# Kernel tuning notes

Measured on AMD Instinct MI355X. Metric: run time of the kernel, lower is better.

## Reference

```python
import jax, jax.numpy as jnp
import numpy as np
import math

R = 16            # input_resolution (window side)
N = R * R         # tokens per window
H = 16            # num_heads
D = 32            # head_dim
SCALE = D ** -0.5

def _rel_pos_index(r):
    # Swin-style relative position index, [N, N] int
    coords = np.stack(np.meshgrid(np.arange(r), np.arange(r), indexing='ij'))  # [2,r,r]
    cf = coords.reshape(2, -1)                          # [2, N]
    rel = cf[:, :, None] - cf[:, None, :]               # [2, N, N]
    rel = rel.transpose(1, 2, 0).astype(np.int64)       # [N, N, 2]
    rel[:, :, 0] += r - 1
    rel[:, :, 1] += r - 1
    rel[:, :, 0] *= 2 * r - 1
    return rel.sum(-1)                                  # [N, N]

def _modulation(n, k):
    # cosine-distance modulation matrix, [n*n, n*n]
    idx = np.arange(n * n)
    rr, cc = idx // n, idx % n
    d = np.sqrt((rr[:, None] - rr[None, :]) ** 2 + (cc[:, None] - cc[None, :]) ** 2)
    T = 4 * (n - 1) * math.sqrt(2)
    f = 2 * math.pi / T
    m = np.exp(np.cos(f * d)) / 2
    if k % n == 0:
        k = k - 1
    bound = m[0, k]
    m = np.where(m < bound, 0.0, m)
    return jnp.asarray(m, jnp.float32)

_REL_IDX = jnp.asarray(_rel_pos_index(R))   # [N, N] int
_MOD = _modulation(R, 3 * R)                 # [N, N] float (eval-mode local modulation)

def setup_inputs() -> dict:
    key = jax.random.key(0)
    ks = jax.random.split(key, 6)
    C = H * D
    return {
        'x': jax.random.normal(ks[0], (128, N, C), jnp.float32),
        'qkv_w': jax.random.normal(ks[1], (3 * C, C), jnp.float32) * 0.02,
        'qkv_b': jax.random.normal(ks[2], (3 * C,), jnp.float32) * 0.02,
        'proj_w': jax.random.normal(ks[3], (C, C), jnp.float32) * 0.02,
        'proj_b': jax.random.normal(ks[4], (C,), jnp.float32) * 0.02,
        'rpb_table': jax.random.normal(ks[5], ((2 * R - 1) ** 2, H), jnp.float32) * 0.02,
    }

def reference(x, qkv_w, qkv_b, proj_w, proj_b, rpb_table):
    B, n, C = x.shape
    # qkv projection: torch Linear is x @ W^T + b
    qkv = x @ qkv_w.T + qkv_b                       # [B, N, 3C]
    qkv = qkv.reshape(B, n, 3, H, D)
    q = qkv[:, :, 0].transpose(0, 2, 1, 3) * SCALE  # [B, H, N, D]
    k = qkv[:, :, 1].transpose(0, 2, 1, 3)
    v = qkv[:, :, 2].transpose(0, 2, 1, 3)
    attn = jnp.einsum('bhnd,bhmd->bhnm', q, k)      # [B, H, N, N]
    bias = rpb_table[_REL_IDX]                      # [N, N, H]
    attn = attn + bias.transpose(2, 0, 1)[None]     # + [1, H, N, N]
    attn = jax.nn.softmax(attn, axis=-1)
    attn = attn * _MOD[None, None]                  # local eval-mode modulation
    out = jnp.einsum('bhnm,bhmd->bhnd', attn, v)    # [B, H, N, D]
    out = out.transpose(0, 2, 1, 3).reshape(B, n, C)
    return out @ proj_w.T + proj_b
```

## Files before the change

kernel.cpp:

```cpp
#include <hip/hip_runtime.h>
#include <hip/hip_bf16.h>

typedef unsigned short u16;
typedef unsigned int u32;
typedef __bf16 bf16x8 __attribute__((ext_vector_type(8)));
typedef float f32x4 __attribute__((ext_vector_type(4)));

#define AS1(p) ((const __attribute__((address_space(1))) void*)(p))
#define AS3(p) ((__attribute__((address_space(3))) void*)(p))

#define TOK   256
#define CDIM  512
#define QKVC  1536
#define LOG2E 1.4426950408889634f
#define QSCALE (0.17677669529663687f * 1.4426950408889634f)

__device__ __forceinline__ u16 f2b(float f) {
  unsigned u = __float_as_uint(f);
  unsigned r = (u + 0x7fffu + ((u >> 16) & 1u)) >> 16;
  return (u16)r;
}
__device__ __forceinline__ u16 f2bc(float f) {
  __bf16 h = (__bf16)f;
  u16 u;
  __builtin_memcpy(&u, &h, 2);
  return u;
}
__device__ __forceinline__ float bf_lo(u32 wd) { return __uint_as_float(wd << 16); }
__device__ __forceinline__ float bf_hi(u32 wd) { return __uint_as_float(wd & 0xffff0000u); }
__device__ __forceinline__ float ex2(float x) {
  float r;
  asm("v_exp_f32 %0, %1" : "=v"(r) : "v"(x));
  return r;
}

__global__ __launch_bounds__(256) void cvt_bf16_kernel(const float* __restrict__ in,
                                                       u16* __restrict__ out, int n) {
  int i = (blockIdx.x * 256 + threadIdx.x) * 8;
  if (i >= n) return;
  float4 a = *(const float4*)(in + i);
  float4 b = *(const float4*)(in + i + 4);
  u16 h[8];
  h[0] = f2b(a.x); h[1] = f2b(a.y); h[2] = f2b(a.z); h[3] = f2b(a.w);
  h[4] = f2b(b.x); h[5] = f2b(b.y); h[6] = f2b(b.z); h[7] = f2b(b.w);
  *(uint4*)(out + i) = *(const uint4*)h;
}

__global__ __launch_bounds__(256) void build_bias2_kernel(const float* __restrict__ rpb,
                                                          u16* __restrict__ bias2) {
  int i = blockIdx.x * 256 + threadIdx.x;
  int tr = i & 63, lane = (i >> 6) & 63, rb = (i >> 12) & 15, h = i >> 16;
  int t = tr >> 2, r = tr & 3;
  int n = rb * 16 + (lane & 15);
  int m = t * 16 + (lane >> 4) * 4 + r;
  int idx = ((n >> 4) - (m >> 4) + 15) * 31 + ((n & 15) - (m & 15) + 15);
  bias2[i] = f2b(rpb[idx * 16 + h] * LOG2E);
}

__global__ __launch_bounds__(256) void build_mod2_kernel(u16* __restrict__ mod2) {
  int i = blockIdx.x * 256 + threadIdx.x;
  int tr = i & 63, lane = (i >> 6) & 63, rb = i >> 12;
  int t = tr >> 2, r = tr & 3;
  int n = rb * 16 + (lane & 15);
  int m = t * 16 + (lane >> 4) * 4 + r;
  int dr = (n >> 4) - (m >> 4), dc = (n & 15) - (m & 15);
  int d2 = dr * dr + dc * dc;
  float val = 0.0f;
  if (d2 <= 229) {
    const float fc = 6.2831853071795864f / (60.0f * 1.4142135623730951f);
    val = expf(cosf(fc * sqrtf((float)d2))) * 0.5f;
  }
  mod2[i] = f2b(val);
}

template<int MODE>
__global__ __launch_bounds__(256) void gemm_bt(const u16* __restrict__ A,
                                               const u16* __restrict__ Bt,
                                               const float* __restrict__ bvec,
                                               u16* __restrict__ oq,
                                               u16* __restrict__ ok,
                                               u16* __restrict__ ov,
                                               float* __restrict__ of) {
  constexpr int K = 512;
  constexpr int NBN = (MODE == 0) ? 12 : 4;
  constexpr int PER_XCD = (MODE == 0) ? 384 : 128;
  __shared__ __align__(16) u16 As[128 * 64];
  __shared__ __align__(16) u16 Bs[128 * 64];
  const int tid = threadIdx.x, lane = tid & 63, w = tid >> 6;
  const int wr = w >> 1, wc = w & 1, lr = lane & 15, lg = lane >> 4;
  const int logical = (blockIdx.x & 7) * PER_XCD + (blockIdx.x >> 3);
  const int bm = (logical / (2 * NBN)) * 2 + (logical & 1);
  const int bn = (logical % (2 * NBN)) >> 1;
  const u16* Ag = A + (size_t)bm * 128 * K;
  const u16* Bg = Bt + (size_t)bn * 128 * K;
  f32x4 acc[4][4];
#pragma unroll
  for (int m = 0; m < 4; ++m)
#pragma unroll
    for (int n = 0; n < 4; ++n) acc[m][n] = (f32x4){0.f, 0.f, 0.f, 0.f};

  for (int k0 = 0; k0 < K; k0 += 64) {
#pragma unroll
    for (int it = 0; it < 4; ++it) {
      int chunk = it * 256 + w * 64 + lane;
      int r = chunk >> 3, kc = chunk & 7;
      int kcs = kc ^ (r & 7);
      __builtin_amdgcn_global_load_lds(AS1(Ag + (size_t)r * K + k0 + kcs * 8),
                                       AS3(As + chunk * 8), 16, 0, 0);
      __builtin_amdgcn_global_load_lds(AS1(Bg + (size_t)r * K + k0 + kcs * 8),
                                       AS3(Bs + chunk * 8), 16, 0, 0);
    }
    __syncthreads();
#pragma unroll
    for (int kk = 0; kk < 2; ++kk) {
      bf16x8 a[4], b[4];
#pragma unroll
      for (int m = 0; m < 4; ++m) {
        int ar = wr * 64 + m * 16 + lr;
        a[m] = *(const bf16x8*)&As[ar * 64 + (((kk * 4 + lg) ^ (lr & 7)) << 3)];
      }
#pragma unroll
      for (int n = 0; n < 4; ++n) {
        int br = wc * 64 + n * 16 + lr;
        b[n] = *(const bf16x8*)&Bs[br * 64 + (((kk * 4 + lg) ^ (lr & 7)) << 3)];
      }
#pragma unroll
      for (int m = 0; m < 4; ++m)
#pragma unroll
        for (int n = 0; n < 4; ++n)
          acc[m][n] = __builtin_amdgcn_mfma_f32_16x16x32_bf16(a[m], b[n], acc[m][n], 0, 0, 0);
    }
    __syncthreads();
  }

  if (MODE == 1) {
#pragma unroll
    for (int m = 0; m < 4; ++m)
#pragma unroll
      for (int n = 0; n < 4; ++n)
#pragma unroll
        for (int r = 0; r < 4; ++r) {
          int row = bm * 128 + wr * 64 + m * 16 + lg * 4 + r;
          int col = bn * 128 + wc * 64 + n * 16 + lr;
          of[(size_t)row * CDIM + col] = acc[m][n][r] + bvec[col];
        }
    return;
  }

  const int typ = bn >> 2;
  const int col0 = bn * 128 + wc * 64;
  const int row0 = bm * 128 + wr * 64;
  char* Tb = (char*)((w < 2 ? As : Bs) + (w & 1) * 4096);

#pragma unroll
  for (int n = 0; n < 4; ++n) {
    float bv = bvec[col0 + n * 16 + lr];
#pragma unroll
    for (int m = 0; m < 4; ++m)
#pragma unroll
      for (int r = 0; r < 4; ++r) {
        float v = acc[m][n][r] + bv;
        if (typ == 0) v *= QSCALE;
        int row_l, col_l;
        if (typ < 2) { row_l = m * 16 + lg * 4 + r; col_l = n * 16 + lr; }
        else         { row_l = n * 16 + lr;         col_l = m * 16 + lg * 4 + r; }
        int byte = row_l * 128 + ((((col_l >> 3) ^ (row_l & 7)) << 4) | ((col_l & 7) << 1));
        *(u16*)(Tb + byte) = f2b(v);
      }
  }
  asm volatile("" ::: "memory");
  if (typ < 2) {
    int tok = row0 + lane;
    int tokb = tok >> 8;
    u16* obase = (typ == 0) ? oq : ok;
#pragma unroll
    for (int G = 0; G < 8; ++G) {
      int hl = G >> 2, q = G & 3;
      uint4 v = *(const uint4*)(Tb + lane * 128 + ((G ^ (lane & 7)) << 4));
      int hh = ((col0 >> 5) & 15) + hl;
      size_t a = ((((size_t)tokb * 16 + hh) * 16 + ((tok >> 4) & 15)) * 64 +
                  ((tok & 15) | (q << 4))) * 8;
      *(uint4*)(obase + a) = v;
    }
  } else {
    int tl0 = row0 & 255, tokb = row0 >> 8;
    int hl = lane >> 5, t = (lane >> 3) & 3, c = lane & 7;
    int hh = ((col0 >> 5) & 15) + hl;
#pragma unroll
    for (int i = 0; i < 8; ++i) {
      int d = i * 4 + t;
      uint4 v = *(const uint4*)(Tb + (hl * 32 + d) * 128 + (c << 4));
      size_t a = (((size_t)tokb * 16 + hh) * 32 + d) * 256 + tl0 + c * 8;
      *(uint4*)(ov + a) = v;
    }
  }
}

__global__ __launch_bounds__(512, 4) void attn_kernel(const u16* __restrict__ qfrag,
                                                      const u16* __restrict__ kfrag,
                                                      const u16* __restrict__ vsw,
                                                      const u16* __restrict__ bias2,
                                                      const u16* __restrict__ mod2,
                                                      u16* __restrict__ attnout) {
  __shared__ __align__(16) u16 SM[24576];
  const int logical = (blockIdx.x & 7) * 512 + (blockIdx.x >> 3);
  const int h = logical >> 8;
  const int b = (logical >> 1) & 127;
  const int qpair = logical & 1;
  const int tid = threadIdx.x, lane = tid & 63, w = tid >> 6;
  const int lr = lane & 15, lg = lane >> 4;
  const int rb = qpair * 8 + w;
  const int bhid = b * 16 + h;

  const u16* kg = kfrag + (size_t)bhid * 8192;
  const u16* vg = vsw + (size_t)bhid * 8192;
#pragma unroll
  for (int it = 0; it < 2; ++it) {
    __builtin_amdgcn_global_load_lds(AS1(kg + (it * 512 + tid) * 8),
                                     AS3(SM + (it * 512 + tid) * 8), 16, 0, 0);
    __builtin_amdgcn_global_load_lds(AS1(vg + (it * 512 + tid) * 8),
                                     AS3(SM + 8192 + (it * 512 + tid) * 8), 16, 0, 0);
  }
  bf16x8 qf = *(const bf16x8*)(qfrag + ((size_t)bhid * 16 + rb) * 512 + lane * 8);
  __syncthreads();

  const u16* bias_base = bias2 + (((size_t)h * 16 + rb) * 64 + lane) * 64;
  const u16* mod_base  = mod2 + ((size_t)rb * 64 + lane) * 64;
  char* Pbase = (char*)SM + 32768 + w * 2048;
  const char* Vb = (const char*)(SM + 8192);

  f32x4 s[16];
#pragma unroll
  for (int q = 0; q < 4; ++q) {
    u32 bw8[8];
    {
      const uint4* bp = (const uint4*)(bias_base + q * 16);
      *(uint4*)&bw8[0] = bp[0]; *(uint4*)&bw8[4] = bp[1];
    }
#pragma unroll
    for (int tl = 0; tl < 4; ++tl) {
      int t = q * 4 + tl;
      bf16x8 kf = *(const bf16x8*)(SM + (t * 64 + lane) * 8);
      f32x4 c;
      c[0] = bf_lo(bw8[tl * 2]);     c[1] = bf_hi(bw8[tl * 2]);
      c[2] = bf_lo(bw8[tl * 2 + 1]); c[3] = bf_hi(bw8[tl * 2 + 1]);
      s[t] = __builtin_amdgcn_mfma_f32_16x16x32_bf16(kf, qf, c, 0, 0, 0);
    }
  }

  float mr0 = s[0][0], mr1 = s[0][1], mr2 = s[0][2], mr3 = s[0][3];
#pragma unroll
  for (int t = 1; t < 16; ++t) {
    mr0 = fmaxf(mr0, s[t][0]); mr1 = fmaxf(mr1, s[t][1]);
    mr2 = fmaxf(mr2, s[t][2]); mr3 = fmaxf(mr3, s[t][3]);
  }
  float mx = fmaxf(fmaxf(mr0, mr1), fmaxf(mr2, mr3));
  mx = fmaxf(mx, __shfl_xor(mx, 16, 64));
  mx = fmaxf(mx, __shfl_xor(mx, 32, 64));
  float s0 = 0.f, s1 = 0.f, s2 = 0.f, s3 = 0.f;
#pragma unroll
  for (int t = 0; t < 16; ++t) {
    s[t][0] = ex2(s[t][0] - mx); s0 += s[t][0];
    s[t][1] = ex2(s[t][1] - mx); s1 += s[t][1];
    s[t][2] = ex2(s[t][2] - mx); s2 += s[t][2];
    s[t][3] = ex2(s[t][3] - mx); s3 += s[t][3];
  }
  float sm = (s0 + s1) + (s2 + s3);
  sm += __shfl_xor(sm, 16, 64);
  sm += __shfl_xor(sm, 32, 64);
  sm = __builtin_amdgcn_rcpf(sm);

  f32x4 o0 = (f32x4){0.f, 0.f, 0.f, 0.f};
  f32x4 o1 = (f32x4){0.f, 0.f, 0.f, 0.f};
#pragma unroll
  for (int q = 0; q < 4; ++q) {
    u32 mw8[8];
    {
      const uint4* mp = (const uint4*)(mod_base + q * 16);
      *(uint4*)&mw8[0] = mp[0]; *(uint4*)&mw8[4] = mp[1];
    }
#pragma unroll
    for (int tl = 0; tl < 4; ++tl) {
      int t = q * 4 + tl;
      u16 pk[4];
#pragma unroll
      for (int r = 0; r < 4; ++r) {
        u32 wd = mw8[tl * 2 + (r >> 1)];
        float mf = (r & 1) ? bf_hi(wd) : bf_lo(wd);
        pk[r] = f2bc(s[t][r] * sm * mf);
      }
      int hi2 = (t * 2 + (lg >> 1)) & 3;
      *(uint2*)(Pbase + ((t >> 1) & 1) * 1024 + ((hi2 << 4) | lr) * 16 + (lg & 1) * 8)
          = *(const uint2*)pk;
    }
    asm volatile("" ::: "memory");
#pragma unroll
    for (int kl = 0; kl < 2; ++kl) {
      bf16x8 pa = *(const bf16x8*)(Pbase + kl * 1024 + lane * 16);
      int cv = ((q * 2 + kl) * 4 + lg) ^ (lr & 7);
      bf16x8 v0 = *(const bf16x8*)(Vb + lr * 512 + cv * 16);
      bf16x8 v1 = *(const bf16x8*)(Vb + (16 + lr) * 512 + cv * 16);
      o0 = __builtin_amdgcn_mfma_f32_16x16x32_bf16(pa, v0, o0, 0, 0, 0);
      o1 = __builtin_amdgcn_mfma_f32_16x16x32_bf16(pa, v1, o1, 0, 0, 0);
    }
    asm volatile("" ::: "memory");
  }

  u16* orow = attnout + (size_t)(b * TOK + rb * 16) * CDIM + h * 32;
#pragma unroll
  for (int r = 0; r < 4; ++r) {
    orow[(size_t)(lg * 4 + r) * CDIM + lr] = f2bc(o0[r]);
    orow[(size_t)(lg * 4 + r) * CDIM + 16 + lr] = f2bc(o1[r]);
  }
}

extern "C" void kernel_launch(void* const* d_in, const int* in_sizes, int n_in,
                              void* d_out, int out_size, void* d_ws, size_t ws_size,
                              hipStream_t stream) {
  const float* x      = (const float*)d_in[0];
  const float* qkv_w  = (const float*)d_in[1];
  const float* qkv_b  = (const float*)d_in[2];
  const float* proj_w = (const float*)d_in[3];
  const float* proj_b = (const float*)d_in[4];
  const float* rpb    = (const float*)d_in[5];

  char* ws = (char*)d_ws;
  u16* xb     = (u16*)(ws);
  u16* qkvwb  = (u16*)(ws + 33554432);
  u16* projwb = (u16*)(ws + 35127296);
  u16* qfrag  = (u16*)(ws + 35651584);
  u16* kfrag  = (u16*)(ws + 69206016);
  u16* vswb   = (u16*)(ws + 102760448);
  u16* attnb  = (u16*)(ws + 136314880);
  u16* bias2  = (u16*)(ws + 169869312);
  u16* mod2   = (u16*)(ws + 171966464);

  cvt_bf16_kernel<<<8192, 256, 0, stream>>>(x, xb, 32768 * 512);
  cvt_bf16_kernel<<<384, 256, 0, stream>>>(qkv_w, qkvwb, 1536 * 512);
  cvt_bf16_kernel<<<128, 256, 0, stream>>>(proj_w, projwb, 512 * 512);
  build_bias2_kernel<<<4096, 256, 0, stream>>>(rpb, bias2);
  build_mod2_kernel<<<256, 256, 0, stream>>>(mod2);

  gemm_bt<0><<<3072, 256, 0, stream>>>(xb, qkvwb, qkv_b, qfrag, kfrag, vswb, nullptr);
  attn_kernel<<<4096, 512, 0, stream>>>(qfrag, kfrag, vswb, bias2, mod2, attnb);
  gemm_bt<1><<<1024, 256, 0, stream>>>(attnb, projwb, proj_b,
                                       nullptr, nullptr, nullptr, (float*)d_out);
}
```

Baseline: 221.1 us.

## Fuse x fp32-to-bf16 conversion into QKV GEMM and enlarge M tile to 256

Removes the separate conversion pass over x by loading fp32 x directly in the QKV GEMM, converting in registers and storing swizzled bf16 into LDS. The QKV GEMM block grows to 512 threads with a 256-row A tile, so each weight tile is reused across twice as many rows. This avoids writing and rereading a 32 MB bf16 copy of x. In exchange, A loads become synchronous register loads instead of async global-to-LDS transfers, which may reduce latency hiding. The epilogue staging layout is also changed for eight waves.

```diff
diff --git a/kernel.cpp b/kernel.cpp
--- a/kernel.cpp
+++ b/kernel.cpp
@@ -74,24 +74,24 @@
 }
 
 template<int MODE>
-__global__ __launch_bounds__(256) void gemm_bt(const u16* __restrict__ A,
-                                               const u16* __restrict__ Bt,
-                                               const float* __restrict__ bvec,
-                                               u16* __restrict__ oq,
-                                               u16* __restrict__ ok,
-                                               u16* __restrict__ ov,
-                                               float* __restrict__ of) {
+__global__ __launch_bounds__(MODE == 0 ? 512 : 256) void gemm_bt(
+    const float* __restrict__ Ax, const u16* __restrict__ A,
+    const u16* __restrict__ Bt, const float* __restrict__ bvec,
+    u16* __restrict__ oq, u16* __restrict__ ok, u16* __restrict__ ov,
+    float* __restrict__ of) {
   constexpr int K = 512;
+  constexpr int BM = (MODE == 0) ? 256 : 128;
+  constexpr int NT = (MODE == 0) ? 512 : 256;
   constexpr int NBN = (MODE == 0) ? 12 : 4;
-  constexpr int PER_XCD = (MODE == 0) ? 384 : 128;
-  __shared__ __align__(16) u16 As[128 * 64];
-  __shared__ __align__(16) u16 Bs[128 * 64];
+  constexpr int PER_XCD = (MODE == 0) ? 192 : 128;
+  __shared__ __align__(16) u16 SM[(MODE == 0) ? 32768 : 16384];
+  u16* As = SM;
+  u16* Bs = SM + BM * 64;
   const int tid = threadIdx.x, lane = tid & 63, w = tid >> 6;
   const int wr = w >> 1, wc = w & 1, lr = lane & 15, lg = lane >> 4;
   const int logical = (blockIdx.x & 7) * PER_XCD + (blockIdx.x >> 3);
   const int bm = (logical / (2 * NBN)) * 2 + (logical & 1);
   const int bn = (logical % (2 * NBN)) >> 1;
-  const u16* Ag = A + (size_t)bm * 128 * K;
   const u16* Bg = Bt + (size_t)bn * 128 * K;
   f32x4 acc[4][4];
 #pragma unroll
@@ -100,15 +100,40 @@
     for (int n = 0; n < 4; ++n) acc[m][n] = (f32x4){0.f, 0.f, 0.f, 0.f};
 
   for (int k0 = 0; k0 < K; k0 += 64) {
-#pragma unroll
-    for (int it = 0; it < 4; ++it) {
-      int chunk = it * 256 + w * 64 + lane;
-      int r = chunk >> 3, kc = chunk & 7;
-      int kcs = kc ^ (r & 7);
-      __builtin_amdgcn_global_load_lds(AS1(Ag + (size_t)r * K + k0 + kcs * 8),
-                                       AS3(As + chunk * 8), 16, 0, 0);
-      __builtin_amdgcn_global_load_lds(AS1(Bg + (size_t)r * K + k0 + kcs * 8),
-                                       AS3(Bs + chunk * 8), 16, 0, 0);
+    if (MODE == 0) {
+#pragma unroll
+      for (int it = 0; it < 4; ++it) {
+        int chunk = it * NT + tid;
+        int r = chunk >> 3, kc = chunk & 7;
+        int gg = kc ^ (r & 7);
+        const float* src = Ax + (size_t)(bm * 256 + r) * K + k0 + gg * 8;
+        float4 v0 = *(const float4*)src;
+        float4 v1 = *(const float4*)(src + 4);
+        u16 hb[8];
+        hb[0] = f2bc(v0.x); hb[1] = f2bc(v0.y); hb[2] = f2bc(v0.z); hb[3] = f2bc(v0.w);
+        hb[4] = f2bc(v1.x); hb[5] = f2bc(v1.y); hb[6] = f2bc(v1.z); hb[7] = f2bc(v1.w);
+        *(uint4*)(As + chunk * 8) = *(const uint4*)hb;
+      }
+#pragma unroll
+      for (int it = 0; it < 2; ++it) {
+        int chunk = it * NT + tid;
+        int r = chunk >> 3, kc = chunk & 7;
+        int kcs = kc ^ (r & 7);
+        __builtin_amdgcn_global_load_lds(AS1(Bg + (size_t)r * K + k0 + kcs * 8),
+                                         AS3(Bs + chunk * 8), 16, 0, 0);
+      }
+    } else {
+      const u16* Ag = A + (size_t)bm * 128 * K;
+#pragma unroll
+      for (int it = 0; it < 4; ++it) {
+        int chunk = it * NT + tid;
+        int r = chunk >> 3, kc = chunk & 7;
+        int kcs = kc ^ (r & 7);
+        __builtin_amdgcn_global_load_lds(AS1(Ag + (size_t)r * K + k0 + kcs * 8),
+                                         AS3(As + chunk * 8), 16, 0, 0);
+        __builtin_amdgcn_global_load_lds(AS1(Bg + (size_t)r * K + k0 + kcs * 8),
+                                         AS3(Bs + chunk * 8), 16, 0, 0);
+      }
     }
     __syncthreads();
 #pragma unroll
@@ -140,7 +165,7 @@
       for (int n = 0; n < 4; ++n)
 #pragma unroll
         for (int r = 0; r < 4; ++r) {
-          int row = bm * 128 + wr * 64 + m * 16 + lg * 4 + r;
+          int row = bm * BM + wr * 64 + m * 16 + lg * 4 + r;
           int col = bn * 128 + wc * 64 + n * 16 + lr;
           of[(size_t)row * CDIM + col] = acc[m][n][r] + bvec[col];
         }
@@ -149,8 +174,8 @@
 
   const int typ = bn >> 2;
   const int col0 = bn * 128 + wc * 64;
-  const int row0 = bm * 128 + wr * 64;
-  char* Tb = (char*)((w < 2 ? As : Bs) + (w & 1) * 4096);
+  const int row0 = bm * 256 + wr * 64;
+  char* Tb = (char*)SM + w * 8192;
 
 #pragma unroll
   for (int n = 0; n < 4; ++n) {
@@ -325,7 +350,6 @@
   const float* rpb    = (const float*)d_in[5];
 
   char* ws = (char*)d_ws;
-  u16* xb     = (u16*)(ws);
   u16* qkvwb  = (u16*)(ws + 33554432);
   u16* projwb = (u16*)(ws + 35127296);
   u16* qfrag  = (u16*)(ws + 35651584);
@@ -335,14 +359,14 @@
   u16* bias2  = (u16*)(ws + 169869312);
   u16* mod2   = (u16*)(ws + 171966464);
 
-  cvt_bf16_kernel<<<8192, 256, 0, stream>>>(x, xb, 32768 * 512);
   cvt_bf16_kernel<<<384, 256, 0, stream>>>(qkv_w, qkvwb, 1536 * 512);
   cvt_bf16_kernel<<<128, 256, 0, stream>>>(proj_w, projwb, 512 * 512);
   build_bias2_kernel<<<4096, 256, 0, stream>>>(rpb, bias2);
   build_mod2_kernel<<<256, 256, 0, stream>>>(mod2);
 
-  gemm_bt<0><<<3072, 256, 0, stream>>>(xb, qkvwb, qkv_b, qfrag, kfrag, vswb, nullptr);
+  gemm_bt<0><<<1536, 512, 0, stream>>>(x, nullptr, qkvwb, qkv_b,
+                                       qfrag, kfrag, vswb, nullptr);
   attn_kernel<<<4096, 512, 0, stream>>>(qfrag, kfrag, vswb, bias2, mod2, attnb);
-  gemm_bt<1><<<1024, 256, 0, stream>>>(attnb, projwb, proj_b,
+  gemm_bt<1><<<1024, 256, 0, stream>>>(nullptr, attnb, projwb, proj_b,
                                        nullptr, nullptr, nullptr, (float*)d_out);
 }
```

Result: faster. 214.6 us, median of 2 (-3.0%).
